# Kernel optimization log

Measured on AMD Instinct MI355X. Metric: run time of the kernel, lower is better.

Reference implementation:

```python
import jax, jax.numpy as jnp
import numpy as np

SHIFT = 1  # module picks random.random()>0.5 -> +/-1; fixed to +1 for determinism


def setup_inputs() -> dict:
    key = jax.random.key(0)
    k1, k2 = jax.random.split(key)
    x = jax.random.normal(k1, (1, 128, 14, 14), dtype=jnp.float32)
    w = jax.random.normal(k2, (32, 3, 128), dtype=jnp.float32)  # [out_c, kernel, in_c]
    return {"x": x, "w": w}


def reference(x, w):
    # roll + reshape + unfold + permute + einsum chain is equivalent to:
    #   circular roll along W, 1D conv along W (k=3, zero pad 1, 128->32, per H row),
    #   circular roll along H.
    xr = jnp.roll(x, SHIFT, axis=3)
    # w[j,k,i] -> OIHW kernel (32, 128, 1, 3); H kernel size 1, W kernel size 3
    kern = jnp.transpose(w, (0, 2, 1))[:, :, None, :]
    y = jax.lax.conv_general_dilated(
        xr, kern,
        window_strides=(1, 1),
        padding=((0, 0), (1, 1)),
        dimension_numbers=("NCHW", "OIHW", "NCHW"),
    )  # (1, 32, 14, 14)
    return jnp.roll(y, SHIFT, axis=2)
```

## Files before the change

### kernel.cpp

```cpp
#include <hip/hip_runtime.h>


__global__ __launch_bounds__(256) void conv_roll_kernel(
    const float* __restrict__ x,
    const float* __restrict__ wt,
    float* __restrict__ out)
{
    const int o = blockIdx.x;
    const int t = threadIdx.x;
    if (t >= 196) return;

    const int h  = t / 14;
    const int w  = t - h * 14;
    const int hh = (h + 13) % 14;
    const int rb = hh * 14;

    const int i0 = rb + ((w + 12) % 14);
    const int i1 = rb + ((w + 13) % 14);
    const int i2 = rb + w;

    const float m0 = (w > 0)  ? 1.0f : 0.0f;
    const float m2 = (w < 13) ? 1.0f : 0.0f;

    const float* __restrict__ wo = wt + o * 384;

    float a0 = 0.0f, a1 = 0.0f, a2 = 0.0f;
#pragma unroll 8
    for (int i = 0; i < 128; ++i) {
        const float* __restrict__ xp = x + i * 196;
        a0 = __builtin_fmaf(xp[i0], wo[i],       a0);
        a1 = __builtin_fmaf(xp[i1], wo[128 + i], a1);
        a2 = __builtin_fmaf(xp[i2], wo[256 + i], a2);
    }

    out[o * 196 + t] = m0 * a0 + a1 + m2 * a2;
}

extern "C" void kernel_launch(void* const* d_in, const int* in_sizes, int n_in,
                              void* d_out, int out_size, void* d_ws, size_t ws_size,
                              hipStream_t stream) {
    const float* x  = (const float*)d_in[0];
    const float* wt = (const float*)d_in[1];
    float* out = (float*)d_out;

    conv_roll_kernel<<<32, 256, 0, stream>>>(x, wt, out);
}
```

Before: 63.20 us.

## Split input-channel reduction across threads with shared-memory reduce, more blocks

Launches one block per (output channel, output row) instead of one per output channel, giving 448 blocks. Inside each block, 16 channel groups of 8 input channels are each handled by 14 threads, which compute partial sums. The partials are then summed through shared memory. This is meant to cut the long serial 128-iteration dependency chain per thread and occupy many more CUs, at the cost of a __syncthreads and a small serial reduction done by 14 threads.

```diff
diff --git a/kernel.cpp b/kernel.cpp
--- a/kernel.cpp
+++ b/kernel.cpp
@@ -6,34 +6,50 @@
     const float* __restrict__ wt,
     float* __restrict__ out)
 {
-    const int o = blockIdx.x;
-    const int t = threadIdx.x;
-    if (t >= 196) return;
+    __shared__ float red[224];
 
-    const int h  = t / 14;
-    const int w  = t - h * 14;
+    const int bx = blockIdx.x;
+    const int o  = bx / 14;
+    const int h  = bx - o * 14;
     const int hh = (h + 13) % 14;
     const int rb = hh * 14;
 
-    const int i0 = rb + ((w + 12) % 14);
-    const int i1 = rb + ((w + 13) % 14);
-    const int i2 = rb + w;
+    const int t = threadIdx.x;
 
-    const float m0 = (w > 0)  ? 1.0f : 0.0f;
-    const float m2 = (w < 13) ? 1.0f : 0.0f;
+    if (t < 224) {
+        const int ci = t / 14;
+        const int w  = t - ci * 14;
 
-    const float* __restrict__ wo = wt + o * 384;
+        const int c0 = rb + ((w + 12) % 14);
+        const int c1 = rb + ((w + 13) % 14);
+        const int c2 = rb + w;
 
-    float a0 = 0.0f, a1 = 0.0f, a2 = 0.0f;
-#pragma unroll 8
-    for (int i = 0; i < 128; ++i) {
-        const float* __restrict__ xp = x + i * 196;
-        a0 = __builtin_fmaf(xp[i0], wo[i],       a0);
-        a1 = __builtin_fmaf(xp[i1], wo[128 + i], a1);
-        a2 = __builtin_fmaf(xp[i2], wo[256 + i], a2);
+        const float* __restrict__ wo = wt + o * 384 + ci * 8;
+        const float* __restrict__ xb = x + (ci * 8) * 196;
+
+        float a0 = 0.f, a1 = 0.f, a2 = 0.f;
+#pragma unroll
+        for (int j = 0; j < 8; ++j) {
+            const float* __restrict__ xp = xb + j * 196;
+            a0 = __builtin_fmaf(xp[c0], wo[j],       a0);
+            a1 = __builtin_fmaf(xp[c1], wo[128 + j], a1);
+            a2 = __builtin_fmaf(xp[c2], wo[256 + j], a2);
+        }
+
+        const float m0 = (w > 0)  ? 1.0f : 0.0f;
+        const float m2 = (w < 13) ? 1.0f : 0.0f;
+        red[t] = m0 * a0 + a1 + m2 * a2;
     }
 
-    out[o * 196 + t] = m0 * a0 + a1 + m2 * a2;
+    __syncthreads();
+
+    if (t < 14) {
+        float s = 0.f;
+#pragma unroll
+        for (int ci = 0; ci < 16; ++ci)
+            s += red[ci * 14 + t];
+        out[o * 196 + h * 14 + t] = s;
+    }
 }
 
 extern "C" void kernel_launch(void* const* d_in, const int* in_sizes, int n_in,
@@ -43,5 +59,5 @@
     const float* wt = (const float*)d_in[1];
     float* out = (float*)d_out;
 
-    conv_roll_kernel<<<32, 256, 0, stream>>>(x, wt, out);
+    conv_roll_kernel<<<448, 256, 0, stream>>>(x, wt, out);
 }
```

Measured after the change: 56.01 us. 11.4% less time.
